# Kernel tuning notes

Measured on AMD Instinct MI355X. Metric: run time of the kernel, lower is better.

The kernel has to match this reference:

```python
import jax, jax.numpy as jnp
import numpy as np

MAX_DEG = 10
MIN_DEG = 0
N_FEAT = 128
NB_FILTER = 128
BATCH = 128
DEG_COUNT = 30000                      # atoms per degree bucket (static)
N_ATOMS = (MAX_DEG + 1) * DEG_COUNT    # 330000, atoms sorted by degree (deg0 first)
NB_AFFINE = 3 * MAX_DEG + (2 - MIN_DEG)  # 32
EPS = 1e-5


def setup_inputs() -> dict:
    key = jax.random.key(0)
    ks = jax.random.split(key, 16)
    atoms = jax.random.normal(ks[0], (N_ATOMS, N_FEAT), dtype=jnp.float32)
    membership = jax.random.randint(ks[1], (N_ATOMS,), 0, BATCH)
    # deg_slice[d] = [start, count] for degree d (atoms sorted by degree)
    deg_slice = jnp.stack([jnp.arange(MAX_DEG + 1) * DEG_COUNT,
                           jnp.full((MAX_DEG + 1,), DEG_COUNT)], axis=1)
    inp = {"atoms": atoms, "deg_slice": deg_slice, "membership": membership}
    for d in range(1, MAX_DEG + 1):
        inp[f"adj{d}"] = jax.random.randint(ks[1 + d], (DEG_COUNT, d), 0, N_ATOMS)
    glorot = (2.0 / (N_FEAT + NB_FILTER)) ** 0.5
    inp["W"] = jax.random.normal(ks[12], (NB_AFFINE, N_FEAT, NB_FILTER), dtype=jnp.float32) * glorot
    inp["b"] = jnp.zeros((NB_AFFINE, NB_FILTER), dtype=jnp.float32)
    inp["gamma"] = jnp.ones((NB_FILTER,), dtype=jnp.float32)
    inp["beta"] = jnp.zeros((NB_FILTER,), dtype=jnp.float32)
    return inp


def _self_slice(atoms, deg):
    return jax.lax.dynamic_slice_in_dim(atoms, deg * DEG_COUNT, DEG_COUNT, axis=0)


def _norm(x, gamma, beta):
    m = jnp.mean(x, axis=-1, keepdims=True)
    std = jnp.sqrt(jnp.var(x, axis=-1, keepdims=True) + EPS)
    return gamma * ((x - m) / (std + EPS)) + beta


def _forward(atoms, W, b, gamma, beta, membership, adjs):
    # W consumption order matches the TF iterator: for deg=1..max_deg -> (rel, self),
    # then deg0 self at index 2*MAX_DEG, then gather affines deg1..max_deg, deg0 last.
    rel_outs = [None] * (MAX_DEG + 1)
    gather_outs = [None] * (MAX_DEG + 1)
    for d in range(1, MAX_DEG + 1):
        neigh = jnp.sum(atoms[adjs[d - 1]], axis=1)          # (COUNT, F) gather+sum
        self_a = _self_slice(atoms, d)                        # (COUNT, F)
        i_rel, i_self = 2 * (d - 1), 2 * d - 1
        rel_outs[d] = (neigh @ W[i_rel] + b[i_rel]) + (self_a @ W[i_self] + b[i_self])
        i_g = 2 * MAX_DEG + d
        gather_outs[d] = self_a @ W[i_g] + b[i_g]
    self0 = _self_slice(atoms, 0)
    rel_outs[0] = self0 @ W[2 * MAX_DEG] + b[2 * MAX_DEG]
    gather_outs[0] = self0 @ W[NB_AFFINE - 1] + b[NB_AFFINE - 1]

    activated = jnp.concatenate(rel_outs, axis=0)             # (N_ATOMS, NB_FILTER)
    gathered = jnp.concatenate(gather_outs, axis=0)           # (N_ATOMS, NB_FILTER)
    # graph_gather: per-molecule sum (dynamic_partition + reduce_sum)
    atom_gather = jax.ops.segment_sum(gathered, membership, num_segments=BATCH)

    xn = _norm(activated, gamma, beta)                        # per-row "BN" as in source
    yn = _norm(atom_gather, gamma, beta)
    # gather_node: per-molecule max of normalized atom features
    g = jax.ops.segment_max(xn, membership, num_segments=BATCH)
    return xn, yn, g


def reference(atoms, deg_slice, membership, adj1, adj2, adj3, adj4, adj5,
              adj6, adj7, adj8, adj9, adj10, W, b, gamma, beta):
    adjs = (adj1, adj2, adj3, adj4, adj5, adj6, adj7, adj8, adj9, adj10)
    return _forward(atoms, W, b, gamma, beta, membership, adjs)
```

## Files before the change

kernel.cpp:

```cpp
#include <hip/hip_runtime.h>
#include <stdint.h>

#define MAX_DEG   10
#define DEG_COUNT 30000
#define N_ATOMS   330000
#define NF        128
#define BATCH     128
#define SORT_BLOCKS 256

typedef __attribute__((ext_vector_type(8))) short bf16x8;
typedef __attribute__((ext_vector_type(4))) float f32x4;
typedef __attribute__((ext_vector_type(2))) float f32x2;

__device__ __forceinline__ float bf2f(unsigned short h) {
  union { unsigned u; float f; } v; v.u = ((unsigned)h) << 16; return v.f;
}
__device__ __forceinline__ unsigned short f2bf(float f) {
  union { float f; unsigned u; } v; v.f = f;
  unsigned u = v.u;
  unsigned r = (u + 0x7fffu + ((u >> 16) & 1u)) >> 16;
  return (unsigned short)r;
}

struct AdjPtrs { const int* p[10]; };

#define NEG_INF_BITS 0xFF800000

__global__ __launch_bounds__(256) void k_cast(const f32x4* __restrict__ src,
                                              ushort4* __restrict__ dst) {
  size_t i = (size_t)blockIdx.x * 256 + threadIdx.x;
  f32x4 v = __builtin_nontemporal_load(src + i);
  ushort4 o;
  o.x = f2bf(v[0]); o.y = f2bf(v[1]); o.z = f2bf(v[2]); o.w = f2bf(v[3]);
  dst[i] = o;
}

__global__ __launch_bounds__(256) void k_build_b(const float* __restrict__ W,
                                                 unsigned short* __restrict__ BcatT) {
  int idx = blockIdx.x * 256 + threadIdx.x;
  if (idx >= 11 * 128 * 256) return;
  int d = idx >> 15;
  int rem = idx & 32767;
  int n = rem >> 8;
  int k = rem & 255;
  float v;
  if (k < 128) {
    v = (d >= 1) ? W[(2 * (d - 1)) * 16384 + k * 128 + n] : 0.f;
  } else {
    int ks = k - 128;
    int wi = (d >= 1) ? (2 * d - 1) : 20;
    v = W[wi * 16384 + ks * 128 + n];
  }
  BcatT[idx] = f2bf(v);
}

__global__ __launch_bounds__(256) void k_build_bias(const float* __restrict__ b,
                                                    float* __restrict__ biascat) {
  int idx = blockIdx.x * 256 + threadIdx.x;
  if (idx >= 11 * 128) return;
  int d = idx >> 7, n = idx & 127;
  float f = (d >= 1) ? (b[(2 * (d - 1)) * 128 + n] + b[(2 * d - 1) * 128 + n])
                     : b[20 * 128 + n];
  biascat[idx] = f;
}

template<int D>
__device__ __forceinline__ void nsum_phase0(const unsigned* __restrict__ atomsU,
                                            const int* __restrict__ abase,
                                            unsigned* __restrict__ NS,
                                            int rowTile, int wave, int lane) {
  for (int it = 0; it < 8; ++it) {
    int iloc = wave * 16 + it * 2;
    int r0 = rowTile * 128 + iloc;
    int sw0 = lane ^ ((iloc & 7) << 2);
    int sw1 = lane ^ (((iloc + 1) & 7) << 2);
    if (r0 < DEG_COUNT - 1) {
      const int* a = abase + (size_t)r0 * D;
      int myIdx = (lane < 2 * D) ? a[lane] : 0;
      unsigned xs[2 * D];
#pragma unroll
      for (int j = 0; j < 2 * D; ++j) {
        int nbr = __shfl(myIdx, j, 64);
        xs[j] = atomsU[(size_t)nbr * 64 + lane];
      }
      float s0a = 0.f, s1a = 0.f, s0b = 0.f, s1b = 0.f;
#pragma unroll
      for (int j = 0; j < D; ++j) {
        s0a += bf2f((unsigned short)(xs[j] & 0xffff));
        s1a += bf2f((unsigned short)(xs[j] >> 16));
      }
#pragma unroll
      for (int j = D; j < 2 * D; ++j) {
        s0b += bf2f((unsigned short)(xs[j] & 0xffff));
        s1b += bf2f((unsigned short)(xs[j] >> 16));
      }
      NS[(size_t)iloc * 64 + sw0]       = (unsigned)f2bf(s0a) | ((unsigned)f2bf(s1a) << 16);
      NS[(size_t)(iloc + 1) * 64 + sw1] = (unsigned)f2bf(s0b) | ((unsigned)f2bf(s1b) << 16);
    } else {
      const int* a = abase + (size_t)(DEG_COUNT - 1) * D;
      int myIdx = (lane < D) ? a[lane] : 0;
      unsigned xs[D];
#pragma unroll
      for (int j = 0; j < D; ++j) {
        int nbr = __shfl(myIdx, j, 64);
        xs[j] = atomsU[(size_t)nbr * 64 + lane];
      }
      float s0 = 0.f, s1 = 0.f;
#pragma unroll
      for (int j = 0; j < D; ++j) {
        s0 += bf2f((unsigned short)(xs[j] & 0xffff));
        s1 += bf2f((unsigned short)(xs[j] >> 16));
      }
      unsigned p = (unsigned)f2bf(s0) | ((unsigned)f2bf(s1) << 16);
      NS[(size_t)iloc * 64 + sw0] = p;
      NS[(size_t)(iloc + 1) * 64 + sw1] = p;
    }
  }
}

__global__ __launch_bounds__(512, 4) void k_gemm(
    const unsigned short* __restrict__ atomsBf,
    AdjPtrs adj,
    const unsigned short* __restrict__ BcatT,
    const float* __restrict__ biascat,
    const float* __restrict__ gamma,
    const float* __restrict__ beta,
    float* __restrict__ out0)
{
  const int d = blockIdx.y;
  const int rowTile = blockIdx.x;
  const int tid = threadIdx.x;
  const int lane = tid & 63;
  const int wave = tid >> 6;
  const int m16 = lane & 15;
  const int g = lane >> 4;

  __shared__ unsigned short Bs[128 * 256];
  unsigned* NS = (unsigned*)Bs;

  const unsigned short* Bd = BcatT + d * 32768;
  const unsigned* atomsU = (const unsigned*)atomsBf;

  const int rowBase = rowTile * 128 + wave * 16;
  bf16x8 af[8];
  {
    int rbL = rowBase + m16; if (rbL > DEG_COUNT - 1) rbL = DEG_COUNT - 1;
    size_t gr = (size_t)d * DEG_COUNT + rbL;
#pragma unroll
    for (int ks = 4; ks < 8; ++ks)
      af[ks] = *(const bf16x8*)(atomsBf + gr * 128 + (ks - 4) * 32 + g * 8);
  }

  if (d > 0) {
    const int* abase = adj.p[d - 1];
    switch (d) {
      case 1:  nsum_phase0<1>(atomsU, abase, NS, rowTile, wave, lane); break;
      case 2:  nsum_phase0<2>(atomsU, abase, NS, rowTile, wave, lane); break;
      case 3:  nsum_phase0<3>(atomsU, abase, NS, rowTile, wave, lane); break;
      case 4:  nsum_phase0<4>(atomsU, abase, NS, rowTile, wave, lane); break;
      case 5:  nsum_phase0<5>(atomsU, abase, NS, rowTile, wave, lane); break;
      case 6:  nsum_phase0<6>(atomsU, abase, NS, rowTile, wave, lane); break;
      case 7:  nsum_phase0<7>(atomsU, abase, NS, rowTile, wave, lane); break;
      case 8:  nsum_phase0<8>(atomsU, abase, NS, rowTile, wave, lane); break;
      case 9:  nsum_phase0<9>(atomsU, abase, NS, rowTile, wave, lane); break;
      default: nsum_phase0<10>(atomsU, abase, NS, rowTile, wave, lane); break;
    }
    __syncthreads();
    const char* nsb = (const char*)NS;
    const int rowb = (wave * 16 + m16) * 256;
    const int sw = (m16 & 7) << 4;
#pragma unroll
    for (int ks = 0; ks < 4; ++ks)
      af[ks] = *(const bf16x8*)(nsb + ((rowb + ks * 64 + g * 16) ^ sw));
    __syncthreads();
  } else {
    bf16x8 z = {0, 0, 0, 0, 0, 0, 0, 0};
#pragma unroll
    for (int ks = 0; ks < 4; ++ks) af[ks] = z;
  }

#pragma unroll
  for (int it = 0; it < 8; ++it) {
    int flat = it * 512 + tid;
    int row = flat >> 5;
    int c = flat & 31;
    uint4 v = *(const uint4*)(Bd + row * 256 + c * 8);
    int kb = (c * 16) ^ ((row & 7) << 4);
    *(uint4*)((char*)Bs + row * 512 + kb) = v;
  }

  __syncthreads();

  const int ldsMask = (m16 & 7) << 4;

  f32x4 acc[8];
#pragma unroll
  for (int ct = 0; ct < 8; ++ct) acc[ct] = (f32x4){0.f, 0.f, 0.f, 0.f};

#pragma unroll
  for (int ct = 0; ct < 8; ++ct) {
    const char* bbase = (const char*)Bs + (ct * 16 + m16) * 512;
    bf16x8 bf[8];
#pragma unroll
    for (int ks = 0; ks < 8; ++ks)
      bf[ks] = *(const bf16x8*)(bbase + ((ks * 64 + g * 16) ^ ldsMask));
#pragma unroll
    for (int ks = 0; ks < 8; ++ks)
      acc[ct] = __builtin_amdgcn_mfma_f32_16x16x32_bf16(af[ks], bf[ks], acc[ct], 0, 0, 0);
  }

  float bias_[8], gam[8], bet[8];
#pragma unroll
  for (int ct = 0; ct < 8; ++ct) {
    bias_[ct] = biascat[d * 128 + ct * 16 + m16];
    gam[ct] = gamma[ct * 16 + m16];
    bet[ct] = beta[ct * 16 + m16];
  }

#pragma unroll
  for (int ct = 0; ct < 8; ++ct)
#pragma unroll
    for (int r = 0; r < 4; ++r) acc[ct][r] += bias_[ct];

  float s[4], qq[4];
#pragma unroll
  for (int r = 0; r < 4; ++r) {
    s[r] = 0.f; qq[r] = 0.f;
#pragma unroll
    for (int ct = 0; ct < 8; ++ct) {
      float v = acc[ct][r];
      s[r] += v; qq[r] += v * v;
    }
  }
#pragma unroll
  for (int off = 8; off >= 1; off >>= 1) {
#pragma unroll
    for (int r = 0; r < 4; ++r) {
      s[r]  += __shfl_xor(s[r],  off, 64);
      qq[r] += __shfl_xor(qq[r], off, 64);
    }
  }

#pragma unroll
  for (int r = 0; r < 4; ++r) {
    int rb = rowBase + g * 4 + r;
    float mean = s[r] * (1.0f / 128.0f);
    float var  = qq[r] * (1.0f / 128.0f) - mean * mean;
    float inv  = 1.0f / (sqrtf(var + 1e-5f) + 1e-5f);
    if (rb < DEG_COUNT) {
      size_t grow = (size_t)d * DEG_COUNT + rb;
#pragma unroll
      for (int ct = 0; ct < 8; ++ct) {
        float v = gam[ct] * ((acc[ct][r] - mean) * inv) + bet[ct];
        __builtin_nontemporal_store(v, out0 + grow * 128 + ct * 16 + m16);
      }
    }
  }
}

__global__ __launch_bounds__(256) void k_hist2(const int* __restrict__ membership,
                                               int* __restrict__ blockHist) {
  __shared__ int bins[BATCH];
  int tid = threadIdx.x;
  if (tid < BATCH) bins[tid] = 0;
  __syncthreads();
  const int chunk = (N_ATOMS + SORT_BLOCKS - 1) / SORT_BLOCKS;
  int lo = blockIdx.x * chunk, hi = min(lo + chunk, N_ATOMS);
  for (int i = lo + tid; i < hi; i += 256)
    atomicAdd(&bins[membership[i]], 1);
  __syncthreads();
  if (tid < BATCH) blockHist[blockIdx.x * BATCH + tid] = bins[tid];
}

__global__ __launch_bounds__(128) void k_scan2(const int* __restrict__ blockHist,
                                               int* __restrict__ off,
                                               int* __restrict__ base,
                                               int* __restrict__ hist) {
  int m = threadIdx.x;
  int tot = 0;
  for (int b = 0; b < SORT_BLOCKS; ++b) tot += blockHist[b * BATCH + m];
  hist[m] = tot;
  __shared__ int t[BATCH];
  t[m] = tot;
  __syncthreads();
  int acc = 0;
  for (int i = 0; i < m; ++i) acc += t[i];
  base[m] = acc;
  int run = acc;
  for (int b = 0; b < SORT_BLOCKS; ++b) {
    off[b * BATCH + m] = run;
    run += blockHist[b * BATCH + m];
  }
}

__global__ __launch_bounds__(256) void k_scatter2(const int* __restrict__ membership,
                                                  const int* __restrict__ off,
                                                  int* __restrict__ perm) {
  __shared__ int bins[BATCH];
  int tid = threadIdx.x;
  if (tid < BATCH) bins[tid] = off[blockIdx.x * BATCH + tid];
  __syncthreads();
  const int chunk = (N_ATOMS + SORT_BLOCKS - 1) / SORT_BLOCKS;
  int lo = blockIdx.x * chunk, hi = min(lo + chunk, N_ATOMS);
  for (int i = lo + tid; i < hi; i += 256) {
    int m = membership[i];
    int pos = atomicAdd(&bins[m], 1);
    perm[pos] = i;
  }
}

__global__ __launch_bounds__(512) void k_mreduce(
    const f32x2* __restrict__ xnV,
    const unsigned* __restrict__ atomsU,
    const int* __restrict__ perm,
    const int* __restrict__ base,
    const int* __restrict__ hist,
    float* __restrict__ Spart,
    int* __restrict__ cntPart,
    float2* __restrict__ pmax4)
{
  const int m = blockIdx.x >> 2;
  const int s = blockIdx.x & 3;
  const int b0 = base[m], cnt = hist[m];
  const int lo = b0 + (cnt * s) / 4;
  const int hi = b0 + (cnt * (s + 1)) / 4;
  const int wave = threadIdx.x >> 6, lane = threadIdx.x & 63;

  __shared__ float S[8][11][128];
  __shared__ int C[8][11];
  __shared__ float2 maxT[8][64];
  for (int e = lane; e < 11 * 128; e += 64) S[wave][e >> 7][e & 127] = 0.f;
  if (lane < 11) C[wave][lane] = 0;
  __syncthreads();

  const float NEG_INF = __int_as_float((int)NEG_INF_BITS);
  float mx0 = NEG_INF, mx1 = NEG_INF;

  for (int i = lo + wave; i < hi; i += 8) {
    int r = perm[i];
    int d = r / DEG_COUNT;
    f32x2 x = __builtin_nontemporal_load(xnV + (size_t)r * 64 + lane);
    unsigned a = __builtin_nontemporal_load(atomsU + (size_t)r * 64 + lane);
    mx0 = fmaxf(mx0, x[0]);
    mx1 = fmaxf(mx1, x[1]);
    S[wave][d][lane]      += bf2f((unsigned short)(a & 0xffff));
    S[wave][d][64 + lane] += bf2f((unsigned short)(a >> 16));
    if (lane == 0) C[wave][d]++;
  }
  maxT[wave][lane] = make_float2(mx0, mx1);
  __syncthreads();

  if (threadIdx.x < 64) {
    int l = threadIdx.x;
    float2 mm = maxT[0][l];
#pragma unroll
    for (int w = 1; w < 8; ++w) {
      float2 b = maxT[w][l]; mm.x = fmaxf(mm.x, b.x); mm.y = fmaxf(mm.y, b.y);
    }
    pmax4[(s * 128 + m) * 64 + l] = mm;
  }
  for (int e = threadIdx.x; e < 11 * 128; e += 512) {
    int d = e >> 7, p = e & 127;
    float t = 0.f;
#pragma unroll
    for (int w = 0; w < 8; ++w) t += S[w][d][p];
    int col = (p < 64) ? (2 * p) : (2 * (p - 64) + 1);
    Spart[(((size_t)s * 128 + m) * 11 + d) * 128 + col] = t;
  }
  if (threadIdx.x < 11) {
    int t = 0;
#pragma unroll
    for (int w = 0; w < 8; ++w) t += C[w][threadIdx.x];
    cntPart[((size_t)s * 128 + m) * 11 + threadIdx.x] = t;
  }
}

__global__ __launch_bounds__(128) void k_ynfinal(
    const float* __restrict__ Spart,
    const int* __restrict__ cntPart,
    const float* __restrict__ W,
    const float* __restrict__ b,
    const float* __restrict__ gamma,
    const float* __restrict__ beta,
    const float* __restrict__ pmax4,
    float* __restrict__ out1,
    float* __restrict__ out2)
{
  int m = blockIdx.x;
  int j = threadIdx.x;

  float g = __int_as_float((int)NEG_INF_BITS);
#pragma unroll
  for (int sl = 0; sl < 4; ++sl)
    g = fmaxf(g, pmax4[(sl * 128 + m) * 128 + j]);
  out2[m * 128 + j] = g;

  __shared__ float Sm[11][128];
  __shared__ float cw[11];
  for (int e = j; e < 11 * 128; e += 128) {
    int d = e >> 7, c = e & 127;
    float t = 0.f;
#pragma unroll
    for (int sl = 0; sl < 4; ++sl)
      t += Spart[(((size_t)sl * 128 + m) * 11 + d) * 128 + c];
    Sm[d][c] = t;
  }
  if (j < 11) {
    int t = 0;
#pragma unroll
    for (int sl = 0; sl < 4; ++sl) t += cntPart[((size_t)sl * 128 + m) * 11 + j];
    cw[j] = (float)t;
  }
  __syncthreads();

  float acc = 0.f;
  for (int d = 0; d < 11; ++d) {
    int wi = (d >= 1) ? (20 + d) : 31;
    const float* Wd = W + wi * 16384;
    float a0 = 0.f, a1 = 0.f, a2 = 0.f, a3 = 0.f;
    for (int k = 0; k < 128; k += 4) {
      a0 += Sm[d][k]     * Wd[k * 128 + j];
      a1 += Sm[d][k + 1] * Wd[(k + 1) * 128 + j];
      a2 += Sm[d][k + 2] * Wd[(k + 2) * 128 + j];
      a3 += Sm[d][k + 3] * Wd[(k + 3) * 128 + j];
    }
    acc += (a0 + a1) + (a2 + a3);
    acc += cw[d] * b[wi * 128 + j];
  }

  float ws_ = acc, wq = acc * acc;
#pragma unroll
  for (int off = 32; off >= 1; off >>= 1) {
    ws_ += __shfl_xor(ws_, off, 64);
    wq  += __shfl_xor(wq, off, 64);
  }
  __shared__ float red[4];
  int wave = j >> 6, lane = j & 63;
  if (lane == 0) { red[wave * 2] = ws_; red[wave * 2 + 1] = wq; }
  __syncthreads();
  float Ssum = red[0] + red[2], Q = red[1] + red[3];
  float mean = Ssum * (1.f / 128.f);
  float var = Q * (1.f / 128.f) - mean * mean;
  float inv = 1.f / (sqrtf(var + 1e-5f) + 1e-5f);
  out1[m * 128 + j] = gamma[j] * ((acc - mean) * inv) + beta[j];
}

extern "C" void kernel_launch(void* const* d_in, const int* in_sizes, int n_in,
                              void* d_out, int out_size, void* d_ws, size_t ws_size,
                              hipStream_t stream) {
  const float* atoms = (const float*)d_in[0];
  const int* membership = (const int*)d_in[2];
  AdjPtrs adj;
  for (int i = 0; i < 10; ++i) adj.p[i] = (const int*)d_in[3 + i];
  const float* W     = (const float*)d_in[13];
  const float* b     = (const float*)d_in[14];
  const float* gamma = (const float*)d_in[15];
  const float* beta  = (const float*)d_in[16];

  char* ws = (char*)d_ws;
  size_t off = 0;
  unsigned short* atomsBf = (unsigned short*)(ws + off); off += (size_t)N_ATOMS * 128 * 2;
  unsigned short* BcatT   = (unsigned short*)(ws + off); off += (size_t)11 * 128 * 256 * 2;
  float* biascat          = (float*)(ws + off);          off += (size_t)11 * 128 * 4;
  int* perm               = (int*)(ws + off);            off += (size_t)N_ATOMS * 4;
  int* hist               = (int*)(ws + off);            off += 512;
  int* base_              = (int*)(ws + off);            off += 512;
  int* blockHist          = (int*)(ws + off);            off += (size_t)SORT_BLOCKS * BATCH * 4;
  int* offTab             = (int*)(ws + off);            off += (size_t)SORT_BLOCKS * BATCH * 4;
  float* Spart            = (float*)(ws + off);          off += (size_t)4 * 128 * 11 * 128 * 4;
  int* cntPart            = (int*)(ws + off);            off += (size_t)4 * 128 * 11 * 4;
  float* pmax4            = (float*)(ws + off);          off += (size_t)4 * 128 * 128 * 4;

  float* out0 = (float*)d_out;
  float* out1 = out0 + (size_t)N_ATOMS * 128;
  float* out2 = out1 + 16384;

  hipLaunchKernelGGL(k_cast, dim3(N_ATOMS * 128 / 4 / 256), dim3(256), 0, stream,
                     (const f32x4*)atoms, (ushort4*)atomsBf);
  hipLaunchKernelGGL(k_build_b, dim3((11 * 128 * 256 + 255) / 256), dim3(256), 0, stream, W, BcatT);
  hipLaunchKernelGGL(k_build_bias, dim3((11 * 128 + 255) / 256), dim3(256), 0, stream, b, biascat);
  hipLaunchKernelGGL(k_hist2, dim3(SORT_BLOCKS), dim3(256), 0, stream, membership, blockHist);
  hipLaunchKernelGGL(k_scan2, dim3(1), dim3(128), 0, stream, blockHist, offTab, base_, hist);
  hipLaunchKernelGGL(k_scatter2, dim3(SORT_BLOCKS), dim3(256), 0, stream, membership, offTab, perm);
  hipLaunchKernelGGL(k_gemm, dim3(236, 11), dim3(512), 0, stream,
                     atomsBf, adj, BcatT, biascat, gamma, beta, out0);
  hipLaunchKernelGGL(k_mreduce, dim3(512), dim3(512), 0, stream,
                     (const f32x2*)out0, (const unsigned*)atomsBf, perm, base_, hist,
                     Spart, cntPart, (float2*)pmax4);
  hipLaunchKernelGGL(k_ynfinal, dim3(128), dim3(128), 0, stream,
                     Spart, cntPart, W, b, gamma, beta, pmax4, out1, out2);
}
```

Before: 552.0 us.

## Replace membership sort with LDS-atomic segment reductions fused into cast

Removes the histogram/scan/scatter counting sort over membership and the sorted-order reduction kernel. The fp32 segment sums per degree and molecule are now computed in LDS with atomics inside the bf16 cast kernel. Segment max runs as a separate streaming pass using order-preserving uint keys and atomicMax. The GEMM grid is flattened with degree as the fastest-varying index, and out0 stores are no longer nontemporal. This trades three launches and random-order row reads for shared-memory atomic contention and larger partial buffers that the final kernel must reduce. The segment sums now use fp32 atoms instead of bf16.

```diff
diff --git a/kernel.cpp b/kernel.cpp
--- a/kernel.cpp
+++ b/kernel.cpp
@@ -6,11 +6,13 @@
 #define N_ATOMS   330000
 #define NF        128
 #define BATCH     128
-#define SORT_BLOCKS 256
+#define SSUM_CHUNKS 24
+#define SSUM_CHUNK  1250
+#define SMAX_BLOCKS 256
+#define SMAX_CHUNK  1290
 
 typedef __attribute__((ext_vector_type(8))) short bf16x8;
 typedef __attribute__((ext_vector_type(4))) float f32x4;
-typedef __attribute__((ext_vector_type(2))) float f32x2;
 
 __device__ __forceinline__ float bf2f(unsigned short h) {
   union { unsigned u; float f; } v; v.u = ((unsigned)h) << 16; return v.f;
@@ -21,18 +23,60 @@
   unsigned r = (u + 0x7fffu + ((u >> 16) & 1u)) >> 16;
   return (unsigned short)r;
 }
+__device__ __forceinline__ unsigned fkey(float f) {
+  unsigned u = __float_as_uint(f);
+  return u ^ ((u & 0x80000000u) ? 0xFFFFFFFFu : 0x80000000u);
+}
+__device__ __forceinline__ float funkey(unsigned k) {
+  unsigned u = (k & 0x80000000u) ? (k ^ 0x80000000u) : ~k;
+  return __uint_as_float(u);
+}
 
 struct AdjPtrs { const int* p[10]; };
 
 #define NEG_INF_BITS 0xFF800000
 
-__global__ __launch_bounds__(256) void k_cast(const f32x4* __restrict__ src,
-                                              ushort4* __restrict__ dst) {
-  size_t i = (size_t)blockIdx.x * 256 + threadIdx.x;
-  f32x4 v = __builtin_nontemporal_load(src + i);
-  ushort4 o;
-  o.x = f2bf(v[0]); o.y = f2bf(v[1]); o.z = f2bf(v[2]); o.w = f2bf(v[3]);
-  dst[i] = o;
+__global__ __launch_bounds__(512) void k_cast_ssum(
+    const float2* __restrict__ atomsV,
+    const int* __restrict__ membership,
+    unsigned* __restrict__ dstU,
+    float* __restrict__ Spart,
+    int* __restrict__ cntPart)
+{
+  __shared__ float S[BATCH * 128];
+  __shared__ int C[BATCH];
+  const int tid = threadIdx.x;
+  const int wave = tid >> 6, lane = tid & 63;
+  const int c = blockIdx.x, d = blockIdx.y;
+  for (int e = tid; e < BATCH * 128; e += 512) S[e] = 0.f;
+  if (tid < BATCH) C[tid] = 0;
+  __syncthreads();
+
+  const int lo = d * DEG_COUNT + c * SSUM_CHUNK;
+  const int hi = lo + SSUM_CHUNK;
+
+  auto doRow = [&](int r) {
+    if (r < hi) {
+      float2 x = atomsV[(size_t)r * 64 + lane];
+      int m = membership[r];
+      dstU[(size_t)r * 64 + lane] = (unsigned)f2bf(x.x) | ((unsigned)f2bf(x.y) << 16);
+      atomicAdd(&S[m * 128 + lane], x.x);
+      atomicAdd(&S[m * 128 + 64 + lane], x.y);
+      if (lane == 0) atomicAdd(&C[m], 1);
+    }
+  };
+  for (int r = lo + wave * 4; r < hi; r += 32) {
+    doRow(r); doRow(r + 1); doRow(r + 2); doRow(r + 3);
+  }
+  __syncthreads();
+
+  float* slice = Spart + (size_t)(d * SSUM_CHUNKS + c) * (BATCH * 128);
+  for (int e = tid; e < BATCH * 128; e += 512) {
+    int p = e & 127;
+    int col = (p < 64) ? (2 * p) : (2 * (p - 64) + 1);
+    slice[(e & ~127) + col] = S[e];
+  }
+  if (tid < BATCH) cntPart[(d * SSUM_CHUNKS + c) * BATCH + tid] = C[tid];
 }
 
 __global__ __launch_bounds__(256) void k_build_b(const float* __restrict__ W,
@@ -127,8 +171,9 @@
     const float* __restrict__ beta,
     float* __restrict__ out0)
 {
-  const int d = blockIdx.y;
-  const int rowTile = blockIdx.x;
+  const int bid = blockIdx.x;
+  const int d = bid % 11;
+  const int rowTile = bid / 11;
   const int tid = threadIdx.x;
   const int lane = tid & 63;
   const int wave = tid >> 6;
@@ -250,165 +295,82 @@
     if (rb < DEG_COUNT) {
       size_t grow = (size_t)d * DEG_COUNT + rb;
 #pragma unroll
-      for (int ct = 0; ct < 8; ++ct) {
-        float v = gam[ct] * ((acc[ct][r] - mean) * inv) + bet[ct];
-        __builtin_nontemporal_store(v, out0 + grow * 128 + ct * 16 + m16);
-      }
-    }
-  }
-}
-
-__global__ __launch_bounds__(256) void k_hist2(const int* __restrict__ membership,
-                                               int* __restrict__ blockHist) {
-  __shared__ int bins[BATCH];
-  int tid = threadIdx.x;
-  if (tid < BATCH) bins[tid] = 0;
-  __syncthreads();
-  const int chunk = (N_ATOMS + SORT_BLOCKS - 1) / SORT_BLOCKS;
-  int lo = blockIdx.x * chunk, hi = min(lo + chunk, N_ATOMS);
-  for (int i = lo + tid; i < hi; i += 256)
-    atomicAdd(&bins[membership[i]], 1);
-  __syncthreads();
-  if (tid < BATCH) blockHist[blockIdx.x * BATCH + tid] = bins[tid];
-}
-
-__global__ __launch_bounds__(128) void k_scan2(const int* __restrict__ blockHist,
-                                               int* __restrict__ off,
-                                               int* __restrict__ base,
-                                               int* __restrict__ hist) {
-  int m = threadIdx.x;
-  int tot = 0;
-  for (int b = 0; b < SORT_BLOCKS; ++b) tot += blockHist[b * BATCH + m];
-  hist[m] = tot;
-  __shared__ int t[BATCH];
-  t[m] = tot;
-  __syncthreads();
-  int acc = 0;
-  for (int i = 0; i < m; ++i) acc += t[i];
-  base[m] = acc;
-  int run = acc;
-  for (int b = 0; b < SORT_BLOCKS; ++b) {
-    off[b * BATCH + m] = run;
-    run += blockHist[b * BATCH + m];
-  }
-}
-
-__global__ __launch_bounds__(256) void k_scatter2(const int* __restrict__ membership,
-                                                  const int* __restrict__ off,
-                                                  int* __restrict__ perm) {
-  __shared__ int bins[BATCH];
-  int tid = threadIdx.x;
-  if (tid < BATCH) bins[tid] = off[blockIdx.x * BATCH + tid];
-  __syncthreads();
-  const int chunk = (N_ATOMS + SORT_BLOCKS - 1) / SORT_BLOCKS;
-  int lo = blockIdx.x * chunk, hi = min(lo + chunk, N_ATOMS);
-  for (int i = lo + tid; i < hi; i += 256) {
-    int m = membership[i];
-    int pos = atomicAdd(&bins[m], 1);
-    perm[pos] = i;
-  }
-}
-
-__global__ __launch_bounds__(512) void k_mreduce(
-    const f32x2* __restrict__ xnV,
-    const unsigned* __restrict__ atomsU,
-    const int* __restrict__ perm,
-    const int* __restrict__ base,
-    const int* __restrict__ hist,
-    float* __restrict__ Spart,
-    int* __restrict__ cntPart,
-    float2* __restrict__ pmax4)
+      for (int ct = 0; ct < 8; ++ct)
+        out0[grow * 128 + ct * 16 + m16] = gam[ct] * ((acc[ct][r] - mean) * inv) + bet[ct];
+    }
+  }
+}
+
+__global__ __launch_bounds__(512) void k_smax(
+    const float2* __restrict__ xnV,
+    const int* __restrict__ membership,
+    unsigned* __restrict__ kmaxPart)
 {
-  const int m = blockIdx.x >> 2;
-  const int s = blockIdx.x & 3;
-  const int b0 = base[m], cnt = hist[m];
-  const int lo = b0 + (cnt * s) / 4;
-  const int hi = b0 + (cnt * (s + 1)) / 4;
-  const int wave = threadIdx.x >> 6, lane = threadIdx.x & 63;
-
-  __shared__ float S[8][11][128];
-  __shared__ int C[8][11];
-  __shared__ float2 maxT[8][64];
-  for (int e = lane; e < 11 * 128; e += 64) S[wave][e >> 7][e & 127] = 0.f;
-  if (lane < 11) C[wave][lane] = 0;
-  __syncthreads();
-
-  const float NEG_INF = __int_as_float((int)NEG_INF_BITS);
-  float mx0 = NEG_INF, mx1 = NEG_INF;
-
-  for (int i = lo + wave; i < hi; i += 8) {
-    int r = perm[i];
-    int d = r / DEG_COUNT;
-    f32x2 x = __builtin_nontemporal_load(xnV + (size_t)r * 64 + lane);
-    unsigned a = __builtin_nontemporal_load(atomsU + (size_t)r * 64 + lane);
-    mx0 = fmaxf(mx0, x[0]);
-    mx1 = fmaxf(mx1, x[1]);
-    S[wave][d][lane]      += bf2f((unsigned short)(a & 0xffff));
-    S[wave][d][64 + lane] += bf2f((unsigned short)(a >> 16));
-    if (lane == 0) C[wave][d]++;
-  }
-  maxT[wave][lane] = make_float2(mx0, mx1);
-  __syncthreads();
-
-  if (threadIdx.x < 64) {
-    int l = threadIdx.x;
-    float2 mm = maxT[0][l];
-#pragma unroll
-    for (int w = 1; w < 8; ++w) {
-      float2 b = maxT[w][l]; mm.x = fmaxf(mm.x, b.x); mm.y = fmaxf(mm.y, b.y);
-    }
-    pmax4[(s * 128 + m) * 64 + l] = mm;
-  }
-  for (int e = threadIdx.x; e < 11 * 128; e += 512) {
-    int d = e >> 7, p = e & 127;
-    float t = 0.f;
-#pragma unroll
-    for (int w = 0; w < 8; ++w) t += S[w][d][p];
+  __shared__ unsigned K[BATCH * 128];
+  const int tid = threadIdx.x;
+  const int wave = tid >> 6, lane = tid & 63;
+  for (int e = tid; e < BATCH * 128; e += 512) K[e] = 0u;
+  __syncthreads();
+
+  const int lo = blockIdx.x * SMAX_CHUNK;
+  const int hi = min(lo + SMAX_CHUNK, N_ATOMS);
+
+  auto doRow = [&](int r) {
+    if (r < hi) {
+      float2 x = xnV[(size_t)r * 64 + lane];
+      int m = membership[r];
+      atomicMax(&K[m * 128 + lane], fkey(x.x));
+      atomicMax(&K[m * 128 + 64 + lane], fkey(x.y));
+    }
+  };
+  for (int r = lo + wave * 4; r < hi; r += 32) {
+    doRow(r); doRow(r + 1); doRow(r + 2); doRow(r + 3);
+  }
+  __syncthreads();
+
+  unsigned* slice = kmaxPart + (size_t)blockIdx.x * (BATCH * 128);
+  for (int e = tid; e < BATCH * 128; e += 512) {
+    int p = e & 127;
     int col = (p < 64) ? (2 * p) : (2 * (p - 64) + 1);
-    Spart[(((size_t)s * 128 + m) * 11 + d) * 128 + col] = t;
-  }
-  if (threadIdx.x < 11) {
-    int t = 0;
-#pragma unroll
-    for (int w = 0; w < 8; ++w) t += C[w][threadIdx.x];
-    cntPart[((size_t)s * 128 + m) * 11 + threadIdx.x] = t;
+    slice[(e & ~127) + col] = K[e];
   }
 }
 
 __global__ __launch_bounds__(128) void k_ynfinal(
     const float* __restrict__ Spart,
     const int* __restrict__ cntPart,
+    const unsigned* __restrict__ kmaxPart,
     const float* __restrict__ W,
     const float* __restrict__ b,
     const float* __restrict__ gamma,
     const float* __restrict__ beta,
-    const float* __restrict__ pmax4,
     float* __restrict__ out1,
     float* __restrict__ out2)
 {
   int m = blockIdx.x;
   int j = threadIdx.x;
 
-  float g = __int_as_float((int)NEG_INF_BITS);
-#pragma unroll
-  for (int sl = 0; sl < 4; ++sl)
-    g = fmaxf(g, pmax4[(sl * 128 + m) * 128 + j]);
-  out2[m * 128 + j] = g;
+  unsigned km = 0u;
+#pragma unroll 4
+  for (int s = 0; s < SMAX_BLOCKS; ++s)
+    km = max(km, kmaxPart[(size_t)s * (BATCH * 128) + m * 128 + j]);
+  out2[m * 128 + j] = (km == 0u) ? __int_as_float((int)NEG_INF_BITS) : funkey(km);
 
   __shared__ float Sm[11][128];
   __shared__ float cw[11];
   for (int e = j; e < 11 * 128; e += 128) {
-    int d = e >> 7, c = e & 127;
+    int d = e >> 7, cix = e & 127;
     float t = 0.f;
-#pragma unroll
-    for (int sl = 0; sl < 4; ++sl)
-      t += Spart[(((size_t)sl * 128 + m) * 11 + d) * 128 + c];
-    Sm[d][c] = t;
+#pragma unroll 4
+    for (int c = 0; c < SSUM_CHUNKS; ++c)
+      t += Spart[(size_t)(d * SSUM_CHUNKS + c) * (BATCH * 128) + m * 128 + cix];
+    Sm[d][cix] = t;
   }
   if (j < 11) {
     int t = 0;
 #pragma unroll
-    for (int sl = 0; sl < 4; ++sl) t += cntPart[((size_t)sl * 128 + m) * 11 + j];
+    for (int c = 0; c < SSUM_CHUNKS; ++c)
+      t += cntPart[(j * SSUM_CHUNKS + c) * BATCH + m];
     cw[j] = (float)t;
   }
   __syncthreads();
@@ -462,31 +424,22 @@
   unsigned short* atomsBf = (unsigned short*)(ws + off); off += (size_t)N_ATOMS * 128 * 2;
   unsigned short* BcatT   = (unsigned short*)(ws + off); off += (size_t)11 * 128 * 256 * 2;
   float* biascat          = (float*)(ws + off);          off += (size_t)11 * 128 * 4;
-  int* perm               = (int*)(ws + off);            off += (size_t)N_ATOMS * 4;
-  int* hist               = (int*)(ws + off);            off += 512;
-  int* base_              = (int*)(ws + off);            off += 512;
-  int* blockHist          = (int*)(ws + off);            off += (size_t)SORT_BLOCKS * BATCH * 4;
-  int* offTab             = (int*)(ws + off);            off += (size_t)SORT_BLOCKS * BATCH * 4;
-  float* Spart            = (float*)(ws + off);          off += (size_t)4 * 128 * 11 * 128 * 4;
-  int* cntPart            = (int*)(ws + off);            off += (size_t)4 * 128 * 11 * 4;
-  float* pmax4            = (float*)(ws + off);          off += (size_t)4 * 128 * 128 * 4;
+  float* Spart            = (float*)(ws + off);          off += (size_t)11 * SSUM_CHUNKS * BATCH * 128 * 4;
+  int* cntPart            = (int*)(ws + off);            off += (size_t)11 * SSUM_CHUNKS * BATCH * 4;
+  unsigned* kmaxPart      = (unsigned*)(ws + off);       off += (size_t)SMAX_BLOCKS * BATCH * 128 * 4;
 
   float* out0 = (float*)d_out;
   float* out1 = out0 + (size_t)N_ATOMS * 128;
   float* out2 = out1 + 16384;
 
-  hipLaunchKernelGGL(k_cast, dim3(N_ATOMS * 128 / 4 / 256), dim3(256), 0, stream,
-                     (const f32x4*)atoms, (ushort4*)atomsBf);
   hipLaunchKernelGGL(k_build_b, dim3((11 * 128 * 256 + 255) / 256), dim3(256), 0, stream, W, BcatT);
   hipLaunchKernelGGL(k_build_bias, dim3((11 * 128 + 255) / 256), dim3(256), 0, stream, b, biascat);
-  hipLaunchKernelGGL(k_hist2, dim3(SORT_BLOCKS), dim3(256), 0, stream, membership, blockHist);
-  hipLaunchKernelGGL(k_scan2, dim3(1), dim3(128), 0, stream, blockHist, offTab, base_, hist);
-  hipLaunchKernelGGL(k_scatter2, dim3(SORT_BLOCKS), dim3(256), 0, stream, membership, offTab, perm);
-  hipLaunchKernelGGL(k_gemm, dim3(236, 11), dim3(512), 0, stream,
+  hipLaunchKernelGGL(k_cast_ssum, dim3(SSUM_CHUNKS, 11), dim3(512), 0, stream,
+                     (const float2*)atoms, membership, (unsigned*)atomsBf, Spart, cntPart);
+  hipLaunchKernelGGL(k_gemm, dim3(236 * 11), dim3(512), 0, stream,
                      atomsBf, adj, BcatT, biascat, gamma, beta, out0);
-  hipLaunchKernelGGL(k_mreduce, dim3(512), dim3(512), 0, stream,
-                     (const f32x2*)out0, (const unsigned*)atomsBf, perm, base_, hist,
-                     Spart, cntPart, (float2*)pmax4);
+  hipLaunchKernelGGL(k_smax, dim3(SMAX_BLOCKS), dim3(512), 0, stream,
+                     (const float2*)out0, membership, kmaxPart);
   hipLaunchKernelGGL(k_ynfinal, dim3(128), dim3(128), 0, stream,
-                     Spart, cntPart, W, b, gamma, beta, pmax4, out1, out2);
-}
+                     Spart, cntPart, kmaxPart, W, b, gamma, beta, out1, out2);
+}
```

Measured after the change: 907.4 us. +64.4%, slower.
